# Kernel tuning notes

Hardware: AMD Instinct MI355X
Metric: run time of the kernel (lower is better)

The kernel has to match this reference:

```python
import jax, jax.numpy as jnp
import numpy as np

N = 100000
E = 1600000
F = 128
COMP_RATIO = 4
K = max(1, N // COMP_RATIO)


def mean_agg(x, src, tgt, n):
    # mean over in-neighbors: h_i = mean_{(j->i) in edges} x_j
    s = jax.ops.segment_sum(x[src], tgt, num_segments=n)          # [N, F]
    cnt = jax.ops.segment_sum(jnp.ones(src.shape[0], x.dtype), tgt, num_segments=n)
    return s / jnp.maximum(cnt, 1.0)[:, None]


def setup_inputs() -> dict:
    key = jax.random.key(0)
    ks = jax.random.split(key, 10)
    sc = 1.0 / np.sqrt(F)
    return {
        "x": jax.random.normal(ks[0], (N, F), jnp.float32),
        "src": jax.random.randint(ks[1], (E,), 0, N, jnp.int32),
        "tgt": jax.random.randint(ks[2], (E,), 0, N, jnp.int32),
        "W_self": jax.random.normal(ks[3], (F, F), jnp.float32) * sc,
        "W_neigh": jax.random.normal(ks[4], (F, F), jnp.float32) * sc,
        "b_pack": jnp.zeros((F,), jnp.float32),
        "w_score": jax.random.normal(ks[5], (F, 1), jnp.float32) * sc,
        "b_score": jnp.zeros((1,), jnp.float32),
        "W_u1": jax.random.normal(ks[6], (F, F), jnp.float32) * sc,
        "b_u1": jnp.zeros((F,), jnp.float32),
        "W_u2": jax.random.normal(ks[7], (F, F), jnp.float32) * sc,
        "b_u2": jnp.zeros((F,), jnp.float32),
    }


def reference(x, src, tgt, W_self, W_neigh, b_pack, w_score, b_score,
              W_u1, b_u1, W_u2, b_u2):
    # ---- compress ----
    # SAGEConv (mean aggregator): fc_self(x) + fc_neigh(mean_neigh(x)) + bias
    h = x @ W_self + mean_agg(x, src, tgt, N) @ W_neigh + b_pack  # [N, F]
    # scorer: Linear(F,1) + Sigmoid
    score = jax.nn.sigmoid(h @ w_score + b_score)[:, 0]           # [N]
    # pool: topk scores, gate selected features by their score
    sel_scores, idx = jax.lax.top_k(score, K)                     # [K], [K]
    new_val = h[idx] * sel_scores[:, None]                        # [K, F]
    # ---- decompress ----
    z = jnp.zeros((N, F), x.dtype).at[idx].set(new_val)
    # diffusion layer 1 (SageConvExt update_func='diffuse'):
    # propagate neighbor mean, keep the received (seed) features fixed
    d = mean_agg(z, src, tgt, N) @ W_u1 + b_u1
    d = d.at[idx].set(z[idx])
    d = jax.nn.relu(d)
    # diffusion layer 2
    out = mean_agg(d, src, tgt, N) @ W_u2 + b_u2
    out = out.at[idx].set(d[idx])
    return out
```

## Files before the change

kernel.cpp:

```cpp
#include <hip/hip_runtime.h>

#define NN 100000
#define NE 1600000
#define FF 128
#define KK 25000
#define NB ((NN + 255) / 256)
#define BM 64
#define BK 32
#define GEMM_GRID ((NN + BM - 1) / BM)

#define BKT_SHIFT 11
#define NPBK (1 << BKT_SHIFT)
#define NBKT2 ((NN + NPBK - 1) >> BKT_SHIFT)
#define NBLKA 512
#define CHUNKA ((NE + NBLKA - 1) / NBLKA)

typedef __attribute__((ext_vector_type(8))) short short8v;
typedef __attribute__((ext_vector_type(4))) float float4v;

__device__ __forceinline__ unsigned short f2b(float f) {
  unsigned u = __float_as_uint(f);
  u += 0x7FFFu + ((u >> 16) & 1u);
  return (unsigned short)(u >> 16);
}
__device__ __forceinline__ unsigned pack2(float lo, float hi) {
  return (unsigned)f2b(lo) | ((unsigned)f2b(hi) << 16);
}

__device__ __forceinline__ unsigned long long topk_key(float s, unsigned i) {
  return (((unsigned long long)__float_as_uint(s)) << 32) |
         (unsigned long long)(0xFFFFFFFFu - i);
}

__global__ __launch_bounds__(256) void k_histA(const int* __restrict__ tgt,
                                               int* __restrict__ histg) {
  __shared__ int h[NBKT2];
  for (int i = threadIdx.x; i < NBKT2; i += 256) h[i] = 0;
  __syncthreads();
  int b = blockIdx.x;
  int e0 = b * CHUNKA, e1 = min(e0 + CHUNKA, NE);
  for (int e = e0 + threadIdx.x; e < e1; e += 256)
    atomicAdd(&h[tgt[e] >> BKT_SHIFT], 1);
  __syncthreads();
  for (int i = threadIdx.x; i < NBKT2; i += 256) histg[i * NBLKA + b] = h[i];
}

__global__ __launch_bounds__(1024) void k_scanA(int* __restrict__ histg,
                                                int* __restrict__ bbase) {
  const int M = NBKT2 * NBLKA;
  const int C = (M + 1023) / 1024;
  __shared__ int part[1024];
  __shared__ int tmp[1024];
  int t = threadIdx.x;
  int i0 = t * C;
  int iend = min(i0 + C, M);
  int s = 0;
  for (int i = i0; i < iend; ++i) s += histg[i];
  part[t] = s;
  __syncthreads();
  int* A = part;
  int* B = tmp;
  for (int off = 1; off < 1024; off <<= 1) {
    int v = A[t] + (t >= off ? A[t - off] : 0);
    B[t] = v;
    __syncthreads();
    int* sw = A; A = B; B = sw;
  }
  int run = (t > 0) ? A[t - 1] : 0;
  for (int i = i0; i < iend; ++i) {
    int v = histg[i];
    histg[i] = run;
    run += v;
  }
  __syncthreads();
  if (t < NBKT2) bbase[t] = histg[t * NBLKA];
  if (t == 0) bbase[NBKT2] = NE;
}

__global__ __launch_bounds__(256) void k_scatterA(const int* __restrict__ src,
                                                  const int* __restrict__ tgt,
                                                  const int* __restrict__ histg,
                                                  int* __restrict__ pairs) {
  __shared__ int cur[NBKT2];
  int b = blockIdx.x;
  for (int i = threadIdx.x; i < NBKT2; i += 256) cur[i] = histg[i * NBLKA + b];
  __syncthreads();
  int e0 = b * CHUNKA, e1 = min(e0 + CHUNKA, NE);
  for (int e = e0 + threadIdx.x; e < e1; e += 256) {
    int t = tgt[e];
    int p = atomicAdd(&cur[t >> BKT_SHIFT], 1);
    pairs[p] = (src[e] << BKT_SHIFT) | (t & (NPBK - 1));
  }
}

__global__ __launch_bounds__(1024) void k_bucketB(const int* __restrict__ pairs,
                                                  const int* __restrict__ bbase,
                                                  int* __restrict__ offsets,
                                                  int* __restrict__ csr) {
  __shared__ int cnt[NPBK];
  __shared__ int part[1024];
  __shared__ int tmp[1024];
  int b = blockIdx.x;
  int t = threadIdx.x;
  int lo = b << BKT_SHIFT;
  int nloc = min(NPBK, NN - lo);
  int base = bbase[b];
  int cntE = bbase[b + 1] - base;
  cnt[t] = 0;
  cnt[t + 1024] = 0;
  __syncthreads();
  for (int p = t; p < cntE; p += 1024)
    atomicAdd(&cnt[pairs[base + p] & (NPBK - 1)], 1);
  __syncthreads();
  int a0 = cnt[2 * t];
  int a1 = cnt[2 * t + 1];
  part[t] = a0 + a1;
  __syncthreads();
  int* A = part;
  int* B = tmp;
  for (int off = 1; off < 1024; off <<= 1) {
    int v = A[t] + (t >= off ? A[t - off] : 0);
    B[t] = v;
    __syncthreads();
    int* sw = A; A = B; B = sw;
  }
  int o0 = (t > 0) ? A[t - 1] : 0;
  int o1 = o0 + a0;
  if (2 * t < nloc) offsets[lo + 2 * t] = base + o0;
  if (2 * t + 1 < nloc) offsets[lo + 2 * t + 1] = base + o1;
  __syncthreads();
  cnt[2 * t] = o0;
  cnt[2 * t + 1] = o1;
  __syncthreads();
  for (int p = t; p < cntE; p += 1024) {
    int v = pairs[base + p];
    int l = v & (NPBK - 1);
    int pos = atomicAdd(&cnt[l], 1);
    csr[base + pos] = v >> BKT_SHIFT;
  }
  if (b == NBKT2 - 1 && t == 0) offsets[NN] = NE;
}

__global__ __launch_bounds__(256) void k_agg(const float* __restrict__ vals,
                                             const int* __restrict__ csr,
                                             const int* __restrict__ offsets,
                                             float* __restrict__ outv) {
  int w = threadIdx.x >> 6;
  int lane = threadIdx.x & 63;
  int half = lane >> 5;
  int li = lane & 31;
  int node = blockIdx.x * 4 + w;
  if (node >= NN) return;
  int beg = offsets[node];
  int end = offsets[node + 1];
  int deg = end - beg;
  float a0 = 0.f, a1 = 0.f, a2 = 0.f, a3 = 0.f;
  int e = beg;
  int e8 = beg + (deg & ~7);
  for (; e < e8; e += 8) {
    float4 v[4];
#pragma unroll
    for (int q = 0; q < 4; ++q) {
      int j = csr[e + 2 * q + half];
      v[q] = *reinterpret_cast<const float4*>(&vals[(size_t)j * FF + li * 4]);
    }
#pragma unroll
    for (int q = 0; q < 4; ++q) {
      a0 += v[q].x; a1 += v[q].y; a2 += v[q].z; a3 += v[q].w;
    }
  }
  for (; e + 2 <= end; e += 2) {
    int j = csr[e + half];
    float4 v = *reinterpret_cast<const float4*>(&vals[(size_t)j * FF + li * 4]);
    a0 += v.x; a1 += v.y; a2 += v.z; a3 += v.w;
  }
  if (e < end && half == 0) {
    int j = csr[e];
    float4 v = *reinterpret_cast<const float4*>(&vals[(size_t)j * FF + li * 4]);
    a0 += v.x; a1 += v.y; a2 += v.z; a3 += v.w;
  }
  a0 += __shfl_xor(a0, 32, 64);
  a1 += __shfl_xor(a1, 32, 64);
  a2 += __shfl_xor(a2, 32, 64);
  a3 += __shfl_xor(a3, 32, 64);
  if (half == 0) {
    float inv = 1.0f / (float)(deg > 0 ? deg : 1);
    *reinterpret_cast<float4*>(&outv[(size_t)node * FF + li * 4]) =
        make_float4(a0 * inv, a1 * inv, a2 * inv, a3 * inv);
  }
}

template <bool GATED>
__global__ __launch_bounds__(256) void k_agg_bf(const unsigned* __restrict__ vals,
                                                const int* __restrict__ csr,
                                                const int* __restrict__ offsets,
                                                const float* __restrict__ sel,
                                                unsigned* __restrict__ outv) {
  int w = threadIdx.x >> 6;
  int lane = threadIdx.x & 63;
  int qt = lane >> 4;
  int li = lane & 15;
  int node = blockIdx.x * 4 + w;
  if (node >= NN) return;
  int beg = offsets[node];
  int end = offsets[node + 1];
  int deg = end - beg;
  float a0 = 0.f, a1 = 0.f, a2 = 0.f, a3 = 0.f;
  float a4 = 0.f, a5 = 0.f, a6 = 0.f, a7 = 0.f;
  int e = beg;
  int e8 = beg + (deg & ~7);
  for (; e < e8; e += 8) {
    uint4 u[2];
#pragma unroll
    for (int q = 0; q < 2; ++q) {
      int j = csr[e + 4 * q + qt];
      u[q] = (!GATED || sel[j] != 0.f)
                 ? *reinterpret_cast<const uint4*>(&vals[(size_t)j * (FF / 2) + li * 4])
                 : make_uint4(0u, 0u, 0u, 0u);
    }
#pragma unroll
    for (int q = 0; q < 2; ++q) {
      a0 += __uint_as_float(u[q].x << 16);
      a1 += __uint_as_float(u[q].x & 0xFFFF0000u);
      a2 += __uint_as_float(u[q].y << 16);
      a3 += __uint_as_float(u[q].y & 0xFFFF0000u);
      a4 += __uint_as_float(u[q].z << 16);
      a5 += __uint_as_float(u[q].z & 0xFFFF0000u);
      a6 += __uint_as_float(u[q].w << 16);
      a7 += __uint_as_float(u[q].w & 0xFFFF0000u);
    }
  }
  for (; e + 4 <= end; e += 4) {
    int j = csr[e + qt];
    uint4 u = (!GATED || sel[j] != 0.f)
                  ? *reinterpret_cast<const uint4*>(&vals[(size_t)j * (FF / 2) + li * 4])
                  : make_uint4(0u, 0u, 0u, 0u);
    a0 += __uint_as_float(u.x << 16);
    a1 += __uint_as_float(u.x & 0xFFFF0000u);
    a2 += __uint_as_float(u.y << 16);
    a3 += __uint_as_float(u.y & 0xFFFF0000u);
    a4 += __uint_as_float(u.z << 16);
    a5 += __uint_as_float(u.z & 0xFFFF0000u);
    a6 += __uint_as_float(u.w << 16);
    a7 += __uint_as_float(u.w & 0xFFFF0000u);
  }
  int r = end - e;
  if (qt < r) {
    int j = csr[e + qt];
    uint4 u = (!GATED || sel[j] != 0.f)
                  ? *reinterpret_cast<const uint4*>(&vals[(size_t)j * (FF / 2) + li * 4])
                  : make_uint4(0u, 0u, 0u, 0u);
    a0 += __uint_as_float(u.x << 16);
    a1 += __uint_as_float(u.x & 0xFFFF0000u);
    a2 += __uint_as_float(u.y << 16);
    a3 += __uint_as_float(u.y & 0xFFFF0000u);
    a4 += __uint_as_float(u.z << 16);
    a5 += __uint_as_float(u.z & 0xFFFF0000u);
    a6 += __uint_as_float(u.w << 16);
    a7 += __uint_as_float(u.w & 0xFFFF0000u);
  }
  a0 += __shfl_xor(a0, 16, 64); a0 += __shfl_xor(a0, 32, 64);
  a1 += __shfl_xor(a1, 16, 64); a1 += __shfl_xor(a1, 32, 64);
  a2 += __shfl_xor(a2, 16, 64); a2 += __shfl_xor(a2, 32, 64);
  a3 += __shfl_xor(a3, 16, 64); a3 += __shfl_xor(a3, 32, 64);
  a4 += __shfl_xor(a4, 16, 64); a4 += __shfl_xor(a4, 32, 64);
  a5 += __shfl_xor(a5, 16, 64); a5 += __shfl_xor(a5, 32, 64);
  a6 += __shfl_xor(a6, 16, 64); a6 += __shfl_xor(a6, 32, 64);
  a7 += __shfl_xor(a7, 16, 64); a7 += __shfl_xor(a7, 32, 64);
  if (qt == 0) {
    float inv = 1.0f / (float)(deg > 0 ? deg : 1);
    uint4 o;
    o.x = pack2(a0 * inv, a1 * inv);
    o.y = pack2(a2 * inv, a3 * inv);
    o.z = pack2(a4 * inv, a5 * inv);
    o.w = pack2(a6 * inv, a7 * inv);
    *reinterpret_cast<uint4*>(&outv[(size_t)node * (FF / 2) + li * 4]) = o;
  }
}

template <int EPI, bool DUAL, bool ABF16>
__global__ __launch_bounds__(256) void k_gemm4(const void* __restrict__ Araw,
                                               const float* __restrict__ W,
                                               const float* __restrict__ A2,
                                               const float* __restrict__ W2,
                                               const float* __restrict__ bias,
                                               const float* __restrict__ aux,
                                               const float* __restrict__ score,
                                               const float* __restrict__ sel,
                                               float* __restrict__ outv,
                                               unsigned* __restrict__ obf,
                                               const float* __restrict__ wsc,
                                               const float* __restrict__ bsc,
                                               float* __restrict__ score_out) {
  __shared__ float As[BK][BM + 4];
  __shared__ float Ws[BK][FF];
  const int tid = threadIdx.x;
  const int tx = tid & 15;
  const int ty = tid >> 4;
  const int m0 = blockIdx.x * BM;

  float acc[4][8];
#pragma unroll
  for (int r = 0; r < 4; ++r)
#pragma unroll
    for (int j = 0; j < 8; ++j) acc[r][j] = 0.f;

  const int NPASS = DUAL ? 2 : 1;
  for (int pass = 0; pass < NPASS; ++pass) {
    const float* Wp = (pass == 0) ? W : W2;
    for (int kt = 0; kt < FF; kt += BK) {
      __syncthreads();
      if (pass == 0 && ABF16) {
        const unsigned* Ab = (const unsigned*)Araw;
#pragma unroll
        for (int t = 0; t < 4; ++t) {
          int i = tid + t * 256;
          int row = i >> 4;
          int cu = i & 15;
          int gr = m0 + row;
          unsigned u = (gr < NN) ? Ab[(size_t)gr * (FF / 2) + (kt >> 1) + cu] : 0u;
          As[cu * 2 + 0][row] = __uint_as_float(u << 16);
          As[cu * 2 + 1][row] = __uint_as_float(u & 0xFFFF0000u);
        }
      } else {
        const float* Ag = (pass == 0) ? (const float*)Araw : A2;
#pragma unroll
        for (int t = 0; t < 2; ++t) {
          int i = tid + t * 256;
          int row = i >> 3;
          int c8 = i & 7;
          int gr = m0 + row;
          float4 v = make_float4(0.f, 0.f, 0.f, 0.f);
          if (gr < NN) v = *(const float4*)&Ag[(size_t)gr * FF + kt + c8 * 4];
          As[c8 * 4 + 0][row] = v.x;
          As[c8 * 4 + 1][row] = v.y;
          As[c8 * 4 + 2][row] = v.z;
          As[c8 * 4 + 3][row] = v.w;
        }
      }
#pragma unroll
      for (int t = 0; t < 4; ++t) {
        int i = tid + t * 256;
        int kr = i >> 5;
        int c4 = i & 31;
        *(float4*)&Ws[kr][c4 * 4] =
            *(const float4*)&Wp[(size_t)(kt + kr) * FF + c4 * 4];
      }
      __syncthreads();
#pragma unroll
      for (int k = 0; k < BK; ++k) {
        float4 a = *(const float4*)&As[k][ty * 4];
        float4 w0 = *(const float4*)&Ws[k][tx * 4];
        float4 w1 = *(const float4*)&Ws[k][tx * 4 + 64];
        float av[4] = {a.x, a.y, a.z, a.w};
        float wv[8] = {w0.x, w0.y, w0.z, w0.w, w1.x, w1.y, w1.z, w1.w};
#pragma unroll
        for (int r = 0; r < 4; ++r)
#pragma unroll
          for (int j = 0; j < 8; ++j) acc[r][j] = fmaf(av[r], wv[j], acc[r][j]);
      }
    }
  }

  float4 b0 = *(const float4*)&bias[tx * 4];
  float4 b1 = *(const float4*)&bias[tx * 4 + 64];
  float bs[8] = {b0.x, b0.y, b0.z, b0.w, b1.x, b1.y, b1.z, b1.w};

  if constexpr (EPI == 0) {
    __shared__ float sp[BM][17];
    float4 s0 = *(const float4*)&wsc[tx * 4];
    float4 s1 = *(const float4*)&wsc[tx * 4 + 64];
    float sv[8] = {s0.x, s0.y, s0.z, s0.w, s1.x, s1.y, s1.z, s1.w};
#pragma unroll
    for (int r = 0; r < 4; ++r) {
      int gi = m0 + ty * 4 + r;
      if (gi >= NN) continue;
      size_t base = (size_t)gi * FF;
      float v[8];
      float p = 0.f;
#pragma unroll
      for (int j = 0; j < 8; ++j) {
        v[j] = acc[r][j] + bs[j];
        p = fmaf(v[j], sv[j], p);
      }
      sp[ty * 4 + r][tx] = p;
      *(float4*)&outv[base + tx * 4] = make_float4(v[0], v[1], v[2], v[3]);
      *(float4*)&outv[base + tx * 4 + 64] = make_float4(v[4], v[5], v[6], v[7]);
    }
    __syncthreads();
    if (tid < BM) {
      int gi = m0 + tid;
      if (gi < NN) {
        float s = 0.f;
#pragma unroll
        for (int t = 0; t < 16; ++t) s += sp[tid][t];
        float z = s + bsc[0];
        score_out[gi] = 1.0f / (1.0f + expf(-z));
      }
    }
  }
}

__global__ __launch_bounds__(256) void k_packW(const float* __restrict__ W,
                                               unsigned* __restrict__ Wpk) {
  int i = blockIdx.x * 256 + threadIdx.x;
  int kt = i >> 9;
  int rem = i & 511;
  int c = rem >> 2;
  int h = rem & 3;
  int kb = kt * 32 + h * 8;
  uint4 o;
  o.x = pack2(W[(kb + 0) * FF + c], W[(kb + 1) * FF + c]);
  o.y = pack2(W[(kb + 2) * FF + c], W[(kb + 3) * FF + c]);
  o.z = pack2(W[(kb + 4) * FF + c], W[(kb + 5) * FF + c]);
  o.w = pack2(W[(kb + 6) * FF + c], W[(kb + 7) * FF + c]);
  *reinterpret_cast<uint4*>(&Wpk[(size_t)i * 4]) = o;
}

template <int EPI>
__global__ __launch_bounds__(256) void k_gemm_mfma(const unsigned* __restrict__ A,
                                                   const unsigned* __restrict__ Wpk,
                                                   const float* __restrict__ bias,
                                                   const float* __restrict__ aux,
                                                   const float* __restrict__ score,
                                                   const float* __restrict__ sel,
                                                   float* __restrict__ outv,
                                                   unsigned short* __restrict__ obf) {
  __shared__ unsigned As[64][68];
  const int tid = threadIdx.x;
  const int wv = tid >> 6;
  const int l = tid & 63;
  const int lg = l >> 4;
  const int lr = l & 15;
  const int m0 = blockIdx.x * 64;

#pragma unroll
  for (int p = 0; p < 4; ++p) {
    int i = tid + p * 256;
    int row = i >> 4, c4 = (i & 15) * 4;
    int gr = m0 + row;
    uint4 v = make_uint4(0u, 0u, 0u, 0u);
    if (gr < NN) v = *reinterpret_cast<const uint4*>(&A[(size_t)gr * 64 + c4]);
    *reinterpret_cast<uint4*>(&As[row][c4]) = v;
  }
  __syncthreads();

  int arow = wv * 16 + lr;
  short8v a[4];
#pragma unroll
  for (int kt = 0; kt < 4; ++kt)
    a[kt] = *reinterpret_cast<const short8v*>(&As[arow][kt * 16 + lg * 4]);

#pragma unroll
  for (int ct = 0; ct < 8; ++ct) {
    float4v acc = {0.f, 0.f, 0.f, 0.f};
    int col = ct * 16 + lr;
#pragma unroll
    for (int kt = 0; kt < 4; ++kt) {
      short8v b = *reinterpret_cast<const short8v*>(
          &Wpk[(size_t)((kt * 128 + col) * 4 + lg) * 4]);
      acc = __builtin_amdgcn_mfma_f32_16x16x32_bf16(a[kt], b, acc, 0, 0, 0);
    }
    float bcol = bias[col];
#pragma unroll
    for (int i = 0; i < 4; ++i) {
      int gi = m0 + wv * 16 + lg * 4 + i;
      if (gi >= NN) continue;
      float g = acc[i] + bcol;
      size_t oi = (size_t)gi * FF + col;
      if (EPI == 1) {
        float se = sel[gi];
        float v;
        if (se != 0.f) {
          v = fmaxf(aux[oi] * score[gi], 0.f);
          outv[oi] = v;
        } else {
          v = fmaxf(g, 0.f);
        }
        obf[(size_t)gi * FF + col] = f2b(v);
      } else {
        float se = sel[gi];
        outv[oi] = (se != 0.f) ? aux[oi] : g;
      }
    }
  }
}

__global__ void k_init_state(unsigned* state) {
  state[0] = 0u;
  state[1] = 0u;
  state[2] = KK;
}

__global__ __launch_bounds__(256) void k_hist(const float* __restrict__ score,
                                              const unsigned* __restrict__ state,
                                              unsigned* __restrict__ hist,
                                              int bits_fixed) {
  __shared__ unsigned lh[256];
  for (int i = threadIdx.x; i < 256; i += 256) lh[i] = 0;
  __syncthreads();
  unsigned long long prefix =
      (((unsigned long long)state[0]) << 32) | (unsigned long long)state[1];
  int i = blockIdx.x * 256 + threadIdx.x;
  if (i < NN) {
    unsigned long long key = topk_key(score[i], (unsigned)i);
    bool ok = (bits_fixed == 0) ? true : (((key ^ prefix) >> (64 - bits_fixed)) == 0ull);
    if (ok) {
      unsigned b = (unsigned)((key >> (56 - bits_fixed)) & 0xFFull);
      atomicAdd(&lh[b], 1u);
    }
  }
  __syncthreads();
  for (int i2 = threadIdx.x; i2 < 256; i2 += 256)
    if (lh[i2]) atomicAdd(&hist[i2], lh[i2]);
}

__global__ __launch_bounds__(256) void k_select_round(unsigned* __restrict__ state,
                                                      unsigned* __restrict__ hist,
                                                      int bits_fixed) {
  __shared__ unsigned h[256];
  int t = threadIdx.x;
  h[t] = hist[t];
  hist[t] = 0;
  __syncthreads();
  if (t == 0) {
    unsigned rem = state[2];
    unsigned long long prefix =
        (((unsigned long long)state[0]) << 32) | (unsigned long long)state[1];
    unsigned cum = 0;
    int bstar = 0;
    for (int b = 255; b >= 0; --b) {
      unsigned c = h[b];
      if (cum + c >= rem) { bstar = b; break; }
      cum += c;
    }
    rem -= cum;
    prefix |= ((unsigned long long)bstar) << (56 - bits_fixed);
    state[0] = (unsigned)(prefix >> 32);
    state[1] = (unsigned)(prefix & 0xFFFFFFFFull);
    state[2] = rem;
  }
}

__global__ __launch_bounds__(256) void k_gate_zg(const float* __restrict__ h,
                                                 const float* __restrict__ score,
                                                 const unsigned* __restrict__ state,
                                                 float* __restrict__ sel,
                                                 unsigned* __restrict__ zg) {
  int w = threadIdx.x >> 6;
  int lane = threadIdx.x & 63;
  int node = blockIdx.x * 4 + w;
  if (node >= NN) return;
  unsigned long long T =
      (((unsigned long long)state[0]) << 32) | (unsigned long long)state[1];
  float s = score[node];
  bool selected = topk_key(s, (unsigned)node) >= T;
  if (lane == 0) sel[node] = selected ? 1.0f : 0.0f;
  if (!selected) return;
  float2 v = *reinterpret_cast<const float2*>(&h[(size_t)node * FF + lane * 2]);
  zg[(size_t)node * (FF / 2) + lane] = pack2(v.x * s, v.y * s);
}

extern "C" void kernel_launch(void* const* d_in, const int* in_sizes, int n_in,
                              void* d_out, int out_size, void* d_ws, size_t ws_size,
                              hipStream_t stream) {
  const float* x = (const float*)d_in[0];
  const int* src = (const int*)d_in[1];
  const int* tgt = (const int*)d_in[2];
  const float* W_self = (const float*)d_in[3];
  const float* W_neigh = (const float*)d_in[4];
  const float* b_pack = (const float*)d_in[5];
  const float* w_score = (const float*)d_in[6];
  const float* b_score = (const float*)d_in[7];
  const float* W_u1 = (const float*)d_in[8];
  const float* b_u1 = (const float*)d_in[9];
  const float* W_u2 = (const float*)d_in[10];
  const float* b_u2 = (const float*)d_in[11];
  float* out = (float*)d_out;

  char* ws = (char*)d_ws;
  size_t off = 0;
  auto alloc = [&](size_t bytes) -> char* {
    char* p = ws + off;
    off += (bytes + 255) & ~(size_t)255;
    return p;
  };
  int* offsets = (int*)alloc((size_t)(NN + 1) * 4);
  int* csr = (int*)alloc((size_t)NE * 4);
  int* histg = (int*)alloc((size_t)NBKT2 * NBLKA * 4);
  int* bbase = (int*)alloc((size_t)(NBKT2 + 1) * 4);
  float* score = (float*)alloc((size_t)NN * 4);
  float* sel = (float*)alloc((size_t)NN * 4);
  unsigned* hist = (unsigned*)alloc(256 * 4);
  unsigned* state = (unsigned*)alloc(64);
  unsigned* pkW1 = (unsigned*)alloc(2048 * 16);
  unsigned* pkW2 = (unsigned*)alloc(2048 * 16);
  float* aggF = (float*)alloc((size_t)NN * FF * 4);
  int* pairs = (int*)aggF;
  unsigned* zdbf = (unsigned*)aggF;
  unsigned* aggBF = (unsigned*)(aggF + (size_t)NN * (FF / 2));
  float* bufB = out;

  hipMemsetAsync(hist, 0, 256 * 4, stream);
  k_init_state<<<1, 1, 0, stream>>>(state);
  k_packW<<<8, 256, 0, stream>>>(W_u1, pkW1);
  k_packW<<<8, 256, 0, stream>>>(W_u2, pkW2);

  k_histA<<<NBLKA, 256, 0, stream>>>(tgt, histg);
  k_scanA<<<1, 1024, 0, stream>>>(histg, bbase);
  k_scatterA<<<NBLKA, 256, 0, stream>>>(src, tgt, histg, pairs);
  k_bucketB<<<NBKT2, 1024, 0, stream>>>(pairs, bbase, offsets, csr);

  k_agg<<<NN / 4, 256, 0, stream>>>(x, csr, offsets, aggF);
  k_gemm4<0, true, false><<<GEMM_GRID, 256, 0, stream>>>(
      aggF, W_neigh, x, W_self, b_pack, nullptr, nullptr, nullptr, bufB, nullptr,
      w_score, b_score, score);

  for (int r = 0; r < 8; ++r) {
    k_hist<<<NB, 256, 0, stream>>>(score, state, hist, 8 * r);
    k_select_round<<<1, 256, 0, stream>>>(state, hist, 8 * r);
  }

  k_gate_zg<<<NN / 4, 256, 0, stream>>>(bufB, score, state, sel, zdbf);
  k_agg_bf<true><<<NN / 4, 256, 0, stream>>>(zdbf, csr, offsets, sel, aggBF);
  k_gemm_mfma<1><<<GEMM_GRID, 256, 0, stream>>>(aggBF, pkW1, b_u1, bufB, score,
                                                sel, bufB,
                                                (unsigned short*)zdbf);
  k_agg_bf<false><<<NN / 4, 256, 0, stream>>>(zdbf, csr, offsets, nullptr, aggBF);
  k_gemm_mfma<2><<<GEMM_GRID, 256, 0, stream>>>(aggBF, pkW2, b_u2, bufB, nullptr,
                                                sel, out, nullptr);
}
```

Before: 573.0 us.

## Shrink top-k radix select to 32-bit keys with tie-break pass

The radix top-k used 64-bit keys (score bits plus inverted index), which took eight histogram/select rounds. It now selects over the 32-bit score bits in four rounds, and the first histogram is built inside the scoring GEMM epilogue. Ties at the threshold are resolved by index with a separate count, scan and mark pass that writes the selection mask. This cuts kernel launches and passes over the scores, but adds three small kernels and global atomics in the GEMM epilogue.

New measurement: 1.232 ms. +115.0%, slower.

```diff
diff --git a/kernel.cpp b/kernel.cpp
--- a/kernel.cpp
+++ b/kernel.cpp
@@ -25,11 +25,6 @@
 }
 __device__ __forceinline__ unsigned pack2(float lo, float hi) {
   return (unsigned)f2b(lo) | ((unsigned)f2b(hi) << 16);
-}
-
-__device__ __forceinline__ unsigned long long topk_key(float s, unsigned i) {
-  return (((unsigned long long)__float_as_uint(s)) << 32) |
-         (unsigned long long)(0xFFFFFFFFu - i);
 }
 
 __global__ __launch_bounds__(256) void k_histA(const int* __restrict__ tgt,
@@ -284,14 +279,11 @@
                                                const float* __restrict__ A2,
                                                const float* __restrict__ W2,
                                                const float* __restrict__ bias,
-                                               const float* __restrict__ aux,
-                                               const float* __restrict__ score,
-                                               const float* __restrict__ sel,
                                                float* __restrict__ outv,
-                                               unsigned* __restrict__ obf,
                                                const float* __restrict__ wsc,
                                                const float* __restrict__ bsc,
-                                               float* __restrict__ score_out) {
+                                               float* __restrict__ score_out,
+                                               unsigned* __restrict__ hist) {
   __shared__ float As[BK][BM + 4];
   __shared__ float Ws[BK][FF];
   const int tid = threadIdx.x;
@@ -395,7 +387,9 @@
 #pragma unroll
         for (int t = 0; t < 16; ++t) s += sp[tid][t];
         float z = s + bsc[0];
-        score_out[gi] = 1.0f / (1.0f + expf(-z));
+        float sc = 1.0f / (1.0f + expf(-z));
+        score_out[gi] = sc;
+        atomicAdd(&hist[__float_as_uint(sc) >> 24], 1u);
       }
     }
   }
@@ -488,8 +482,7 @@
 
 __global__ void k_init_state(unsigned* state) {
   state[0] = 0u;
-  state[1] = 0u;
-  state[2] = KK;
+  state[1] = KK;
 }
 
 __global__ __launch_bounds__(256) void k_hist(const float* __restrict__ score,
@@ -497,22 +490,19 @@
                                               unsigned* __restrict__ hist,
                                               int bits_fixed) {
   __shared__ unsigned lh[256];
-  for (int i = threadIdx.x; i < 256; i += 256) lh[i] = 0;
-  __syncthreads();
-  unsigned long long prefix =
-      (((unsigned long long)state[0]) << 32) | (unsigned long long)state[1];
+  lh[threadIdx.x] = 0;
+  __syncthreads();
+  unsigned prefix = state[0];
   int i = blockIdx.x * 256 + threadIdx.x;
   if (i < NN) {
-    unsigned long long key = topk_key(score[i], (unsigned)i);
-    bool ok = (bits_fixed == 0) ? true : (((key ^ prefix) >> (64 - bits_fixed)) == 0ull);
-    if (ok) {
-      unsigned b = (unsigned)((key >> (56 - bits_fixed)) & 0xFFull);
+    unsigned bits = __float_as_uint(score[i]);
+    if (((bits ^ prefix) >> (32 - bits_fixed)) == 0u) {
+      unsigned b = (bits >> (24 - bits_fixed)) & 0xFFu;
       atomicAdd(&lh[b], 1u);
     }
   }
   __syncthreads();
-  for (int i2 = threadIdx.x; i2 < 256; i2 += 256)
-    if (lh[i2]) atomicAdd(&hist[i2], lh[i2]);
+  if (lh[threadIdx.x]) atomicAdd(&hist[threadIdx.x], lh[threadIdx.x]);
 }
 
 __global__ __launch_bounds__(256) void k_select_round(unsigned* __restrict__ state,
@@ -524,9 +514,8 @@
   hist[t] = 0;
   __syncthreads();
   if (t == 0) {
-    unsigned rem = state[2];
-    unsigned long long prefix =
-        (((unsigned long long)state[0]) << 32) | (unsigned long long)state[1];
+    unsigned rem = state[1];
+    unsigned prefix = state[0];
     unsigned cum = 0;
     int bstar = 0;
     for (int b = 255; b >= 0; --b) {
@@ -535,28 +524,88 @@
       cum += c;
     }
     rem -= cum;
-    prefix |= ((unsigned long long)bstar) << (56 - bits_fixed);
-    state[0] = (unsigned)(prefix >> 32);
-    state[1] = (unsigned)(prefix & 0xFFFFFFFFull);
-    state[2] = rem;
+    prefix |= ((unsigned)bstar) << (24 - bits_fixed);
+    state[0] = prefix;
+    state[1] = rem;
+  }
+}
+
+__global__ __launch_bounds__(256) void k_eqcount(const float* __restrict__ score,
+                                                 const unsigned* __restrict__ state,
+                                                 int* __restrict__ eqc) {
+  __shared__ int s[256];
+  int i = blockIdx.x * 256 + threadIdx.x;
+  unsigned T = state[0];
+  int eq = (i < NN && __float_as_uint(score[i]) == T) ? 1 : 0;
+  s[threadIdx.x] = eq;
+  __syncthreads();
+  for (int off = 128; off > 0; off >>= 1) {
+    if (threadIdx.x < off) s[threadIdx.x] += s[threadIdx.x + off];
+    __syncthreads();
+  }
+  if (threadIdx.x == 0) eqc[blockIdx.x] = s[0];
+}
+
+__global__ __launch_bounds__(512) void k_eqscan(const int* __restrict__ eqc,
+                                                int* __restrict__ eqoff) {
+  __shared__ int s[512];
+  __shared__ int tmp[512];
+  int t = threadIdx.x;
+  int own = (t < NB) ? eqc[t] : 0;
+  s[t] = own;
+  __syncthreads();
+  int* A = s;
+  int* B = tmp;
+  for (int off = 1; off < 512; off <<= 1) {
+    int v = A[t] + (t >= off ? A[t - off] : 0);
+    B[t] = v;
+    __syncthreads();
+    int* sw = A; A = B; B = sw;
+  }
+  if (t < NB) eqoff[t] = A[t] - own;
+}
+
+__global__ __launch_bounds__(256) void k_tb(const float* __restrict__ score,
+                                            const unsigned* __restrict__ state,
+                                            const int* __restrict__ eqoff,
+                                            float* __restrict__ sel) {
+  __shared__ int s[256];
+  __shared__ int tmp[256];
+  int blk = blockIdx.x;
+  int i = blk * 256 + threadIdx.x;
+  unsigned T = state[0];
+  unsigned rem = state[1];
+  unsigned bits = (i < NN) ? __float_as_uint(score[i]) : 0u;
+  int eq = (i < NN && bits == T) ? 1 : 0;
+  s[threadIdx.x] = eq;
+  __syncthreads();
+  int* A = s;
+  int* B = tmp;
+  for (int off = 1; off < 256; off <<= 1) {
+    int v = A[threadIdx.x] + (threadIdx.x >= off ? A[threadIdx.x - off] : 0);
+    B[threadIdx.x] = v;
+    __syncthreads();
+    int* sw = A; A = B; B = sw;
+  }
+  int excl = A[threadIdx.x] - eq;
+  if (i < NN) {
+    float sv = 0.f;
+    if (bits > T) sv = 1.f;
+    else if (eq && (unsigned)(eqoff[blk] + excl) < rem) sv = 1.f;
+    sel[i] = sv;
   }
 }
 
 __global__ __launch_bounds__(256) void k_gate_zg(const float* __restrict__ h,
                                                  const float* __restrict__ score,
-                                                 const unsigned* __restrict__ state,
-                                                 float* __restrict__ sel,
+                                                 const float* __restrict__ sel,
                                                  unsigned* __restrict__ zg) {
   int w = threadIdx.x >> 6;
   int lane = threadIdx.x & 63;
   int node = blockIdx.x * 4 + w;
   if (node >= NN) return;
-  unsigned long long T =
-      (((unsigned long long)state[0]) << 32) | (unsigned long long)state[1];
+  if (sel[node] == 0.f) return;
   float s = score[node];
-  bool selected = topk_key(s, (unsigned)node) >= T;
-  if (lane == 0) sel[node] = selected ? 1.0f : 0.0f;
-  if (!selected) return;
   float2 v = *reinterpret_cast<const float2*>(&h[(size_t)node * FF + lane * 2]);
   zg[(size_t)node * (FF / 2) + lane] = pack2(v.x * s, v.y * s);
 }
@@ -593,6 +642,8 @@
   float* sel = (float*)alloc((size_t)NN * 4);
   unsigned* hist = (unsigned*)alloc(256 * 4);
   unsigned* state = (unsigned*)alloc(64);
+  int* eqc = (int*)alloc((size_t)NB * 4);
+  int* eqoff = (int*)alloc((size_t)NB * 4);
   unsigned* pkW1 = (unsigned*)alloc(2048 * 16);
   unsigned* pkW2 = (unsigned*)alloc(2048 * 16);
   float* aggF = (float*)alloc((size_t)NN * FF * 4);
@@ -613,15 +664,18 @@
 
   k_agg<<<NN / 4, 256, 0, stream>>>(x, csr, offsets, aggF);
   k_gemm4<0, true, false><<<GEMM_GRID, 256, 0, stream>>>(
-      aggF, W_neigh, x, W_self, b_pack, nullptr, nullptr, nullptr, bufB, nullptr,
-      w_score, b_score, score);
-
-  for (int r = 0; r < 8; ++r) {
+      aggF, W_neigh, x, W_self, b_pack, bufB, w_score, b_score, score, hist);
+
+  k_select_round<<<1, 256, 0, stream>>>(state, hist, 0);
+  for (int r = 1; r < 4; ++r) {
     k_hist<<<NB, 256, 0, stream>>>(score, state, hist, 8 * r);
     k_select_round<<<1, 256, 0, stream>>>(state, hist, 8 * r);
   }
-
-  k_gate_zg<<<NN / 4, 256, 0, stream>>>(bufB, score, state, sel, zdbf);
+  k_eqcount<<<NB, 256, 0, stream>>>(score, state, eqc);
+  k_eqscan<<<1, 512, 0, stream>>>(eqc, eqoff);
+  k_tb<<<NB, 256, 0, stream>>>(score, state, eqoff, sel);
+
+  k_gate_zg<<<NN / 4, 256, 0, stream>>>(bufB, score, sel, zdbf);
   k_agg_bf<true><<<NN / 4, 256, 0, stream>>>(zdbf, csr, offsets, sel, aggBF);
   k_gemm_mfma<1><<<GEMM_GRID, 256, 0, stream>>>(aggBF, pkW1, b_u1, bufB, score,
                                                 sel, bufB,
```
